# Kernel optimization log

Hardware: AMD Instinct MI355X
Metric: run time of the kernel (lower is better)

Reference implementation:

```python
import jax, jax.numpy as jnp
import numpy as np

B, R, T, Q = 4096, 130, 200, 64  # batch, ROIs, BOLD length (= feature_nums), query dim
EPS = 1e-5
GCN_DIMS = [(T, 16), (16, 16), (16, 4), (4, 4), (4, 2), (2, 2)]


def bn1d(x, g, b):
    # torch.nn.BatchNorm1d(R) on (B, R, L): channel dim=1, training-mode batch stats, biased var
    m = x.mean(axis=(0, 2), keepdims=True)
    v = ((x - m) ** 2).mean(axis=(0, 2), keepdims=True)
    return g[None, :, None] * (x - m) * jax.lax.rsqrt(v + EPS) + b[None, :, None]


def setup_inputs() -> dict:
    key = jax.random.key(0)
    ks = jax.random.split(key, 16)

    def kaiming(k, shape, fan_in):  # kaiming_normal_ with relu gain
        return (jax.random.normal(k, shape) * np.sqrt(2.0 / fan_in)).astype(jnp.float32)

    inp = {}
    inp['BOLD_signals'] = jax.random.normal(ks[0], (B, R, T), dtype=jnp.float32)
    inp['threshold'] = jnp.float32(0.005)
    inp['wq'] = kaiming(ks[1], (Q, T), T)
    inp['bq'] = jnp.zeros((Q,), jnp.float32)
    inp['g_t'] = jnp.ones((R,), jnp.float32)
    inp['b_t'] = jnp.zeros((R,), jnp.float32)
    for i, (fi, fo) in enumerate(GCN_DIMS, 1):
        inp[f'w{i}'] = kaiming(ks[1 + i], (fo, fi), fi)
        inp[f'b{i}'] = jnp.zeros((fo,), jnp.float32)
        inp[f'g{i}'] = jnp.ones((R,), jnp.float32)
        inp[f'beta{i}'] = jnp.zeros((R,), jnp.float32)
    inp['w_mlp'] = kaiming(ks[9], (2, R * 2), R * 2)
    inp['b_mlp'] = jnp.zeros((2,), jnp.float32)
    return inp


def reference(BOLD_signals, threshold, wq, bq, g_t, b_t,
              w1, b1, g1, beta1, w2, b2, g2, beta2, w3, b3, g3, beta3,
              w4, b4, g4, beta4, w5, b5, g5, beta5, w6, b6, g6, beta6,
              w_mlp, b_mlp):
    x = jnp.where(jnp.isnan(BOLD_signals), 0.0, BOLD_signals)  # (B,R,T)

    # Transformer-style relation matrix (note: K is a reshape, not a transpose, per source)
    qk = x @ wq.T + bq                      # (B,R,Q)
    Qm = qk.reshape(-1, R, Q)               # (B,R,Q)
    Km = qk.reshape(-1, Q, R)               # (B,Q,R)  -- faithful reshape
    rel = jnp.einsum('brq,bqs->brs', Qm, Km)  # (B,R,R)
    rel = bn1d(rel, g_t, b_t)
    rel = jax.nn.softmax(rel, axis=2)
    rel = jax.nn.relu(rel - threshold)

    def gcn(A, f, w, b, g, beta):
        return jax.nn.relu(bn1d(A @ f @ w.T + b, g, beta))

    h = gcn(rel, x, w1, b1, g1, beta1)           # (B,R,16)
    h = gcn(rel, h, w2, b2, g2, beta2) + h       # res
    h = gcn(rel, h, w3, b3, g3, beta3)           # (B,R,4)
    h = gcn(rel, h, w4, b4, g4, beta4) + h       # res
    h = gcn(rel, h, w5, b5, g5, beta5)           # (B,R,2)
    h = gcn(rel, h, w6, b6, g6, beta6) + h       # res

    out = jax.nn.relu(h.reshape(h.shape[0], -1) @ w_mlp.T + b_mlp)  # (B,2)
    return out
```

## Files before the change

### kernel.cpp

```cpp
#include <hip/hip_runtime.h>
#include <math.h>


typedef _Float16 f16;
typedef _Float16 f16x8 __attribute__((ext_vector_type(8)));
typedef _Float16 f16x4 __attribute__((ext_vector_type(4)));
typedef float f32x4 __attribute__((ext_vector_type(4)));

#define MFMA16(a, b, c) __builtin_amdgcn_mfma_f32_16x16x32_f16((a), (b), (c), 0, 0, 0)

__global__ __launch_bounds__(256) void k_in(
    const float* __restrict__ x, const float* __restrict__ wq,
    const float* __restrict__ w1, const float* __restrict__ bq,
    f16* __restrict__ qk, f16* __restrict__ xw1)
{
  __shared__ f16 xs[64 * 224];
  __shared__ f16 ws[80 * 224];
  const int tid = threadIdx.x;
  const size_t m0 = (size_t)blockIdx.x * 64;
  for (int i = tid; i < 192; i += 256) {
    int r = i / 3, j = i - (i / 3) * 3;
    *(float4*)&xs[r * 224 + 200 + j * 8] = make_float4(0, 0, 0, 0);
  }
  for (int i = tid; i < 240; i += 256) {
    int r = i / 3, j = i - (i / 3) * 3;
    *(float4*)&ws[r * 224 + 200 + j * 8] = make_float4(0, 0, 0, 0);
  }
  const float4* xsrc = (const float4*)(x + m0 * 200);
  for (int i = tid; i < 3200; i += 256) {
    int r = i / 50, c = i - (i / 50) * 50;
    float4 v = xsrc[i];
    v.x = (v.x != v.x) ? 0.f : v.x;
    v.y = (v.y != v.y) ? 0.f : v.y;
    v.z = (v.z != v.z) ? 0.f : v.z;
    v.w = (v.w != v.w) ? 0.f : v.w;
    f16x4 h; h[0] = (f16)v.x; h[1] = (f16)v.y; h[2] = (f16)v.z; h[3] = (f16)v.w;
    *(f16x4*)&xs[r * 224 + c * 4] = h;
  }
  for (int i = tid; i < 4000; i += 256) {
    int f = i / 50, c = i - (i / 50) * 50;
    const float4* src = (f < 64) ? (const float4*)(wq + f * 200) + c
                                 : (const float4*)(w1 + (f - 64) * 200) + c;
    float4 v = *src;
    f16x4 h; h[0] = (f16)v.x; h[1] = (f16)v.y; h[2] = (f16)v.z; h[3] = (f16)v.w;
    *(f16x4*)&ws[f * 224 + c * 4] = h;
  }
  __syncthreads();
  const int lane = tid & 63, wv = tid >> 6;
  const int mrow = lane & 15, quad = lane >> 4;
  f32x4 acc[5];
#pragma unroll
  for (int n = 0; n < 5; n++) acc[n] = (f32x4){0.f, 0.f, 0.f, 0.f};
  const f16* xrow = &xs[(wv * 16 + mrow) * 224 + quad * 8];
#pragma unroll
  for (int k0 = 0; k0 < 224; k0 += 32) {
    f16x8 af = *(const f16x8*)(xrow + k0);
#pragma unroll
    for (int n = 0; n < 5; n++) {
      f16x8 bf = *(const f16x8*)&ws[(n * 16 + mrow) * 224 + k0 + quad * 8];
      acc[n] = MFMA16(af, bf, acc[n]);
    }
  }
  const size_t rbase = m0 + wv * 16;
#pragma unroll
  for (int n = 0; n < 4; n++) {
    int col = n * 16 + mrow;
    float bqv = bq[col];
#pragma unroll
    for (int i = 0; i < 4; i++)
      qk[(rbase + quad * 4 + i) * 64 + col] = (f16)(acc[n][i] + bqv);
  }
#pragma unroll
  for (int i = 0; i < 4; i++)
    xw1[(rbase + quad * 4 + i) * 16 + mrow] = (f16)acc[4][i];
}

__device__ __forceinline__ void stage_qkt(const f16* qb, f16* Qm, f16* Kt, int tid)
{
  for (int i = tid; i < 1040; i += 256) {
    int r = i >> 3, j = i & 7;
    *(f16x8*)&Qm[r * 72 + j * 8] = *(const f16x8*)(qb + i * 8);
  }
  for (int i = tid; i < 126; i += 256) {
    int r = 130 + i / 9, j = i - (i / 9) * 9;
    *(float4*)&Qm[r * 72 + j * 8] = make_float4(0, 0, 0, 0);
    *(float4*)&Kt[r * 72 + j * 8] = make_float4(0, 0, 0, 0);
  }
  for (int i = tid; i < 8320; i += 256) {
    int q = i / 130, s = i - (i / 130) * 130;
    Kt[s * 72 + q] = qb[i];
  }
}

__global__ __launch_bounds__(256) void k_relstats(
    const f16* __restrict__ qk, float* __restrict__ sp)
{
  __shared__ f16 Qm[144 * 72];
  __shared__ f16 Kt[144 * 72];
  const int b = blockIdx.x, tid = threadIdx.x;
  stage_qkt(qk + (size_t)b * 8320, Qm, Kt, tid);
  __syncthreads();
  const int lane = tid & 63, wv = tid >> 6, mrow = lane & 15, quad = lane >> 4;
  for (int m = wv; m < 9; m += 4) {
    float p1[4] = {0, 0, 0, 0}, p2[4] = {0, 0, 0, 0};
    const f16* arow = &Qm[(m * 16 + mrow) * 72 + quad * 8];
    f16x8 af0 = *(const f16x8*)arow;
    f16x8 af1 = *(const f16x8*)(arow + 32);
    for (int n = 0; n < 9; n++) {
      const f16* brow = &Kt[(n * 16 + mrow) * 72 + quad * 8];
      f32x4 acc = (f32x4){0.f, 0.f, 0.f, 0.f};
      acc = MFMA16(af0, *(const f16x8*)brow, acc);
      acc = MFMA16(af1, *(const f16x8*)(brow + 32), acc);
#pragma unroll
      for (int i = 0; i < 4; i++) { float v = acc[i]; p1[i] += v; p2[i] += v * v; }
    }
#pragma unroll
    for (int i = 0; i < 4; i++)
#pragma unroll
      for (int msk = 1; msk <= 8; msk <<= 1) {
        p1[i] += __shfl_xor(p1[i], msk); p2[i] += __shfl_xor(p2[i], msk);
      }
    if (mrow == 0) {
#pragma unroll
      for (int i = 0; i < 4; i++) {
        int r = m * 16 + quad * 4 + i;
        if (r < 130) {
          sp[(size_t)r * 4096 + b] = p1[i];
          sp[130 * 4096 + (size_t)r * 4096 + b] = p2[i];
        }
      }
    }
  }
}

__global__ __launch_bounds__(256) void k_stats(
    const float* __restrict__ sp, const float* __restrict__ g,
    const float* __restrict__ beta, float invN, float* __restrict__ ac)
{
  const int r = blockIdx.x, tid = threadIdx.x;
  float s1 = 0.f, s2 = 0.f;
  const float* p1 = sp + (size_t)r * 4096;
  const float* p2 = sp + 130 * 4096 + (size_t)r * 4096;
  for (int j = tid; j < 4096; j += 256) { s1 += p1[j]; s2 += p2[j]; }
#pragma unroll
  for (int m = 1; m <= 32; m <<= 1) { s1 += __shfl_xor(s1, m); s2 += __shfl_xor(s2, m); }
  __shared__ float r1[4], r2[4];
  if ((tid & 63) == 0) { r1[tid >> 6] = s1; r2[tid >> 6] = s2; }
  __syncthreads();
  if (tid == 0) {
    float S1 = r1[0] + r1[1] + r1[2] + r1[3];
    float S2 = r2[0] + r2[1] + r2[2] + r2[3];
    float mean = S1 * invN;
    float var = S2 * invN - mean * mean;
    float a = g[r] * rsqrtf(var + 1e-5f);
    ac[r] = a;
    ac[130 + r] = beta[r] - mean * a;
  }
}

__global__ __launch_bounds__(256) void k_Asoft(
    const f16* __restrict__ qk, const float* __restrict__ ac0,
    const float* __restrict__ thrp, f16* __restrict__ A16)
{
  __shared__ f16 Qm[144 * 72];
  __shared__ f16 Kt[144 * 72];
  const int b = blockIdx.x, tid = threadIdx.x;
  stage_qkt(qk + (size_t)b * 8320, Qm, Kt, tid);
  __syncthreads();
  const float thr = *thrp;
  const int lane = tid & 63, wv = tid >> 6, mrow = lane & 15, quad = lane >> 4;
  f16* Ab = A16 + (size_t)b * 17680;
  for (int m = wv; m < 9; m += 4) {
    float a4[4], c4[4];
#pragma unroll
    for (int i = 0; i < 4; i++) {
      int r = m * 16 + quad * 4 + i;
      a4[i] = (r < 130) ? ac0[r] : 0.f;
      c4[i] = (r < 130) ? ac0[130 + r] : 0.f;
    }
    const f16* arow = &Qm[(m * 16 + mrow) * 72 + quad * 8];
    f16x8 af0 = *(const f16x8*)arow;
    f16x8 af1 = *(const f16x8*)(arow + 32);
    float mx[4] = {-3e38f, -3e38f, -3e38f, -3e38f}, sm[4] = {0, 0, 0, 0};
    for (int n = 0; n < 9; n++) {
      const f16* brow = &Kt[(n * 16 + mrow) * 72 + quad * 8];
      f32x4 acc = (f32x4){0.f, 0.f, 0.f, 0.f};
      acc = MFMA16(af0, *(const f16x8*)brow, acc);
      acc = MFMA16(af1, *(const f16x8*)(brow + 32), acc);
      const bool valid = (n * 16 + mrow) < 130;
#pragma unroll
      for (int i = 0; i < 4; i++) {
        float v = a4[i] * acc[i] + c4[i];
        float ve = valid ? v : -3e38f;
        float nm = fmaxf(mx[i], ve);
        sm[i] = sm[i] * __expf(mx[i] - nm) + (valid ? __expf(v - nm) : 0.f);
        mx[i] = nm;
      }
    }
#pragma unroll
    for (int i = 0; i < 4; i++) {
#pragma unroll
      for (int msk = 1; msk <= 8; msk <<= 1) {
        float om = __shfl_xor(mx[i], msk), os = __shfl_xor(sm[i], msk);
        float nm = fmaxf(mx[i], om);
        sm[i] = sm[i] * __expf(mx[i] - nm) + os * __expf(om - nm);
        mx[i] = nm;
      }
      sm[i] = 1.f / sm[i];
    }
    for (int n = 0; n < 9; n++) {
      const f16* brow = &Kt[(n * 16 + mrow) * 72 + quad * 8];
      f32x4 acc = (f32x4){0.f, 0.f, 0.f, 0.f};
      acc = MFMA16(af0, *(const f16x8*)brow, acc);
      acc = MFMA16(af1, *(const f16x8*)(brow + 32), acc);
      const int col = n * 16 + mrow;
#pragma unroll
      for (int i = 0; i < 4; i++) {
        int r = m * 16 + quad * 4 + i;
        if (r < 130) {
          if (col < 130) {
            float v = a4[i] * acc[i] + c4[i];
            float Av = fmaxf(__expf(v - mx[i]) * sm[i] - thr, 0.f);
            Ab[r * 136 + col] = (f16)Av;
          } else if (col < 136) {
            Ab[r * 136 + col] = (f16)0.f;
          }
        }
      }
    }
  }
}

template <int FI, int FO, bool RES, bool G1>
__global__ __launch_bounds__(256) void k_gcn(
    const f16* __restrict__ A16, const float* __restrict__ ZP,
    const float* __restrict__ ZQ, const f16* __restrict__ xw1,
    const float* __restrict__ acP, const float* __restrict__ acQ,
    const float* __restrict__ wmat, const float* __restrict__ bb,
    float* __restrict__ Zout, float* __restrict__ sp)
{
  __shared__ f16 Ald[144 * 160];
  __shared__ f16 gT[16 * 160];
  const int b = blockIdx.x, tid = threadIdx.x;
  const f16* Ab = A16 + (size_t)b * 17680;
  for (int i = tid; i < 2210; i += 256) {
    int r = i / 17, c8 = i - (i / 17) * 17;
    *(f16x8*)&Ald[r * 160 + c8 * 8] = *(const f16x8*)(Ab + r * 136 + c8 * 8);
  }
  for (int i = tid; i < 432; i += 256) {
    int r = i / 3, j = i - (i / 3) * 3;
    *(float4*)&Ald[r * 160 + 136 + j * 8] = make_float4(0, 0, 0, 0);
  }
  for (int i = tid; i < 320; i += 256)
    ((float4*)gT)[i] = make_float4(0, 0, 0, 0);
  __syncthreads();
  if constexpr (G1) {
    for (int i = tid; i < 2080; i += 256) {
      int s = i >> 4, f = i & 15;
      gT[f * 160 + s] = xw1[(size_t)b * 2080 + i];
    }
  } else {
    if (tid < 130) {
      const int r = tid;
      float h[FI];
      const float* zp = ZP + ((size_t)b * 130 + r) * FI;
      const float aP = acP[r], cP = acP[130 + r];
#pragma unroll
      for (int i = 0; i < FI; i++) h[i] = fmaxf(aP * zp[i] + cP, 0.f);
      if constexpr (RES) {
        const float* zq = ZQ + ((size_t)b * 130 + r) * FI;
        const float aQ = acQ[r], cQ = acQ[130 + r];
#pragma unroll
        for (int i = 0; i < FI; i++) h[i] += fmaxf(aQ * zq[i] + cQ, 0.f);
      }
#pragma unroll
      for (int k = 0; k < FO; k++) {
        float s = 0.f;
#pragma unroll
        for (int i = 0; i < FI; i++) s += h[i] * wmat[k * FI + i];
        gT[k * 160 + r] = (f16)s;
      }
    }
  }
  __syncthreads();
  const int lane = tid & 63, wv = tid >> 6, mrow = lane & 15, quad = lane >> 4;
  for (int m = wv; m < 9; m += 4) {
    f32x4 acc = (f32x4){0.f, 0.f, 0.f, 0.f};
    const f16* arow = &Ald[(m * 16 + mrow) * 160];
    const f16* brow = &gT[mrow * 160];
#pragma unroll
    for (int k0 = 0; k0 < 160; k0 += 32) {
      f16x8 af = *(const f16x8*)(arow + k0 + quad * 8);
      f16x8 bf = *(const f16x8*)(brow + k0 + quad * 8);
      acc = MFMA16(af, bf, acc);
    }
    const int col = mrow;
    const float bk = (col < FO) ? bb[col] : 0.f;
    float p1[4], p2[4];
#pragma unroll
    for (int i = 0; i < 4; i++) {
      int r = m * 16 + quad * 4 + i;
      float v = (col < FO) ? acc[i] + bk : 0.f;
      if (col < FO && r < 130)
        Zout[((size_t)b * 130 + r) * FO + col] = v;
      p1[i] = v; p2[i] = v * v;
    }
#pragma unroll
    for (int i = 0; i < 4; i++)
#pragma unroll
      for (int msk = 1; msk <= 8; msk <<= 1) {
        p1[i] += __shfl_xor(p1[i], msk); p2[i] += __shfl_xor(p2[i], msk);
      }
    if (mrow == 0) {
#pragma unroll
      for (int i = 0; i < 4; i++) {
        int r = m * 16 + quad * 4 + i;
        if (r < 130) {
          sp[(size_t)r * 4096 + b] = p1[i];
          sp[130 * 4096 + (size_t)r * 4096 + b] = p2[i];
        }
      }
    }
  }
}

__global__ __launch_bounds__(256) void k_mlp(
    const float* __restrict__ Z5, const float* __restrict__ Z6,
    const float* __restrict__ ac5, const float* __restrict__ ac6,
    const float* __restrict__ wm, const float* __restrict__ bm, float* __restrict__ out)
{
  const int tid = threadIdx.x, lane = tid & 63, wv = tid >> 6;
  const int b = blockIdx.x * 4 + wv;
  const float* z5 = Z5 + (size_t)b * 260;
  const float* z6 = Z6 + (size_t)b * 260;
  float p0 = 0.f, p1 = 0.f;
#pragma unroll
  for (int j = 0; j < 5; j++) {
    int i = lane + 64 * j;
    if (i < 260) {
      int r = i >> 1;
      float h = fmaxf(ac6[r] * z6[i] + ac6[130 + r], 0.f)
              + fmaxf(ac5[r] * z5[i] + ac5[130 + r], 0.f);
      p0 += h * wm[i];
      p1 += h * wm[260 + i];
    }
  }
#pragma unroll
  for (int m = 1; m <= 32; m <<= 1) { p0 += __shfl_xor(p0, m); p1 += __shfl_xor(p1, m); }
  if (lane == 0) {
    out[(size_t)b * 2] = fmaxf(p0 + bm[0], 0.f);
    out[(size_t)b * 2 + 1] = fmaxf(p1 + bm[1], 0.f);
  }
}

extern "C" void kernel_launch(void* const* d_in, const int* in_sizes, int n_in,
                              void* d_out, int out_size, void* d_ws, size_t ws_size,
                              hipStream_t stream) {
  const float* X   = (const float*)d_in[0];
  const float* THR = (const float*)d_in[1];
  const float* WQ  = (const float*)d_in[2];
  const float* BQ  = (const float*)d_in[3];
  const float* GT  = (const float*)d_in[4];
  const float* BT  = (const float*)d_in[5];
  const float* W1 = (const float*)d_in[6];  const float* Bb1 = (const float*)d_in[7];
  const float* G1g = (const float*)d_in[8]; const float* BE1 = (const float*)d_in[9];
  const float* W2 = (const float*)d_in[10]; const float* Bb2 = (const float*)d_in[11];
  const float* G2 = (const float*)d_in[12]; const float* BE2 = (const float*)d_in[13];
  const float* W3 = (const float*)d_in[14]; const float* Bb3 = (const float*)d_in[15];
  const float* G3 = (const float*)d_in[16]; const float* BE3 = (const float*)d_in[17];
  const float* W4 = (const float*)d_in[18]; const float* Bb4 = (const float*)d_in[19];
  const float* G4 = (const float*)d_in[20]; const float* BE4 = (const float*)d_in[21];
  const float* W5 = (const float*)d_in[22]; const float* Bb5 = (const float*)d_in[23];
  const float* G5 = (const float*)d_in[24]; const float* BE5 = (const float*)d_in[25];
  const float* W6 = (const float*)d_in[26]; const float* Bb6 = (const float*)d_in[27];
  const float* G6 = (const float*)d_in[28]; const float* BE6 = (const float*)d_in[29];
  const float* WM = (const float*)d_in[30]; const float* BM = (const float*)d_in[31];

  float* ws = (float*)d_ws;
  f16*   A16   = (f16*)ws;
  f16*   qk16  = (f16*)(ws + 36208640);
  f16*   xw116 = (f16*)(ws + 53248000);
  float* Z1 = ws + 57507840;
  float* Z2 = ws + 66027520;
  float* Z3 = ws + 74547200;
  float* Z4 = ws + 76677120;
  float* Z5 = ws + 78807040;
  float* Z6 = ws + 79872000;
  float* sp = ws + 80936960;
  float* ac = ws + 82001920;

  k_in<<<8320, 256, 0, stream>>>(X, WQ, W1, BQ, qk16, xw116);
  k_relstats<<<4096, 256, 0, stream>>>(qk16, sp);
  k_stats<<<130, 256, 0, stream>>>(sp, GT, BT, 1.f / 532480.f, ac);
  k_Asoft<<<4096, 256, 0, stream>>>(qk16, ac, THR, A16);
  k_gcn<16, 16, false, true><<<4096, 256, 0, stream>>>(A16, nullptr, nullptr, xw116,
      nullptr, nullptr, nullptr, Bb1, Z1, sp);
  k_stats<<<130, 256, 0, stream>>>(sp, G1g, BE1, 1.f / 65536.f, ac + 260);
  k_gcn<16, 16, false, false><<<4096, 256, 0, stream>>>(A16, Z1, nullptr, nullptr,
      ac + 260, nullptr, W2, Bb2, Z2, sp);
  k_stats<<<130, 256, 0, stream>>>(sp, G2, BE2, 1.f / 65536.f, ac + 520);
  k_gcn<16, 4, true, false><<<4096, 256, 0, stream>>>(A16, Z2, Z1, nullptr,
      ac + 520, ac + 260, W3, Bb3, Z3, sp);
  k_stats<<<130, 256, 0, stream>>>(sp, G3, BE3, 1.f / 16384.f, ac + 780);
  k_gcn<4, 4, false, false><<<4096, 256, 0, stream>>>(A16, Z3, nullptr, nullptr,
      ac + 780, nullptr, W4, Bb4, Z4, sp);
  k_stats<<<130, 256, 0, stream>>>(sp, G4, BE4, 1.f / 16384.f, ac + 1040);
  k_gcn<4, 2, true, false><<<4096, 256, 0, stream>>>(A16, Z4, Z3, nullptr,
      ac + 1040, ac + 780, W5, Bb5, Z5, sp);
  k_stats<<<130, 256, 0, stream>>>(sp, G5, BE5, 1.f / 8192.f, ac + 1300);
  k_gcn<2, 2, false, false><<<4096, 256, 0, stream>>>(A16, Z5, nullptr, nullptr,
      ac + 1300, nullptr, W6, Bb6, Z6, sp);
  k_stats<<<130, 256, 0, stream>>>(sp, G6, BE6, 1.f / 8192.f, ac + 1560);
  k_mlp<<<1024, 256, 0, stream>>>(Z5, Z6, ac + 1300, ac + 1560, WM, BM, (float*)d_out);
}
```

Baseline: 1.248 ms.

## Pre-convert weights once, drop redundant LDS staging across kernels

```diff
diff --git a/kernel.cpp b/kernel.cpp
--- a/kernel.cpp
+++ b/kernel.cpp
@@ -9,22 +9,28 @@
 
 #define MFMA16(a, b, c) __builtin_amdgcn_mfma_f32_16x16x32_f16((a), (b), (c), 0, 0, 0)
 
+__global__ __launch_bounds__(256) void w_prep(
+    const float* __restrict__ wq, const float* __restrict__ w1, f16* __restrict__ wf)
+{
+  const int f = blockIdx.x;
+  const int k = threadIdx.x;
+  if (k < 224) {
+    float v = 0.f;
+    if (k < 200) v = (f < 64) ? wq[f * 200 + k] : w1[(f - 64) * 200 + k];
+    wf[f * 224 + k] = (f16)v;
+  }
+}
+
 __global__ __launch_bounds__(256) void k_in(
-    const float* __restrict__ x, const float* __restrict__ wq,
-    const float* __restrict__ w1, const float* __restrict__ bq,
-    f16* __restrict__ qk, f16* __restrict__ xw1)
-{
-  __shared__ f16 xs[64 * 224];
-  __shared__ f16 ws[80 * 224];
+    const float* __restrict__ x, const f16* __restrict__ wf,
+    const float* __restrict__ bq, f16* __restrict__ qk, f16* __restrict__ xw1)
+{
+  __shared__ f16 xs[64 * 232];
   const int tid = threadIdx.x;
   const size_t m0 = (size_t)blockIdx.x * 64;
-  for (int i = tid; i < 192; i += 256) {
-    int r = i / 3, j = i - (i / 3) * 3;
-    *(float4*)&xs[r * 224 + 200 + j * 8] = make_float4(0, 0, 0, 0);
-  }
-  for (int i = tid; i < 240; i += 256) {
-    int r = i / 3, j = i - (i / 3) * 3;
-    *(float4*)&ws[r * 224 + 200 + j * 8] = make_float4(0, 0, 0, 0);
+  {
+    int r = tid >> 2, j = tid & 3;
+    *(float4*)&xs[r * 232 + 200 + j * 8] = make_float4(0, 0, 0, 0);
   }
   const float4* xsrc = (const float4*)(x + m0 * 200);
   for (int i = tid; i < 3200; i += 256) {
@@ -35,15 +41,7 @@
     v.z = (v.z != v.z) ? 0.f : v.z;
     v.w = (v.w != v.w) ? 0.f : v.w;
     f16x4 h; h[0] = (f16)v.x; h[1] = (f16)v.y; h[2] = (f16)v.z; h[3] = (f16)v.w;
-    *(f16x4*)&xs[r * 224 + c * 4] = h;
-  }
-  for (int i = tid; i < 4000; i += 256) {
-    int f = i / 50, c = i - (i / 50) * 50;
-    const float4* src = (f < 64) ? (const float4*)(wq + f * 200) + c
-                                 : (const float4*)(w1 + (f - 64) * 200) + c;
-    float4 v = *src;
-    f16x4 h; h[0] = (f16)v.x; h[1] = (f16)v.y; h[2] = (f16)v.z; h[3] = (f16)v.w;
-    *(f16x4*)&ws[f * 224 + c * 4] = h;
+    *(f16x4*)&xs[r * 232 + c * 4] = h;
   }
   __syncthreads();
   const int lane = tid & 63, wv = tid >> 6;
@@ -51,15 +49,14 @@
   f32x4 acc[5];
 #pragma unroll
   for (int n = 0; n < 5; n++) acc[n] = (f32x4){0.f, 0.f, 0.f, 0.f};
-  const f16* xrow = &xs[(wv * 16 + mrow) * 224 + quad * 8];
+  const f16* xrow = &xs[(wv * 16 + mrow) * 232 + quad * 8];
+  const f16* wrow = wf + mrow * 224 + quad * 8;
 #pragma unroll
   for (int k0 = 0; k0 < 224; k0 += 32) {
     f16x8 af = *(const f16x8*)(xrow + k0);
 #pragma unroll
-    for (int n = 0; n < 5; n++) {
-      f16x8 bf = *(const f16x8*)&ws[(n * 16 + mrow) * 224 + k0 + quad * 8];
-      acc[n] = MFMA16(af, bf, acc[n]);
-    }
+    for (int n = 0; n < 5; n++)
+      acc[n] = MFMA16(af, *(const f16x8*)(wrow + n * 3584 + k0), acc[n]);
   }
   const size_t rbase = m0 + wv * 16;
 #pragma unroll
@@ -75,42 +72,48 @@
     xw1[(rbase + quad * 4 + i) * 16 + mrow] = (f16)acc[4][i];
 }
 
-__device__ __forceinline__ void stage_qkt(const f16* qb, f16* Qm, f16* Kt, int tid)
-{
-  for (int i = tid; i < 1040; i += 256) {
-    int r = i >> 3, j = i & 7;
-    *(f16x8*)&Qm[r * 72 + j * 8] = *(const f16x8*)(qb + i * 8);
-  }
-  for (int i = tid; i < 126; i += 256) {
-    int r = 130 + i / 9, j = i - (i / 9) * 9;
-    *(float4*)&Qm[r * 72 + j * 8] = make_float4(0, 0, 0, 0);
-    *(float4*)&Kt[r * 72 + j * 8] = make_float4(0, 0, 0, 0);
-  }
-  for (int i = tid; i < 8320; i += 256) {
-    int q = i / 130, s = i - (i / 130) * 130;
-    Kt[s * 72 + q] = qb[i];
+__device__ __forceinline__ void gather_bfrags(const f16* qf, int mrow, int quad,
+                                              f16x8 bf[9][2])
+{
+#pragma unroll
+  for (int n = 0; n < 9; n++) {
+    const int s = n * 16 + mrow;
+    const bool ok = (s < 130);
+#pragma unroll
+    for (int kh = 0; kh < 2; kh++) {
+      f16x8 t;
+#pragma unroll
+      for (int j = 0; j < 8; j++) {
+        int q = kh * 32 + quad * 8 + j;
+        t[j] = ok ? qf[q * 130 + s] : (f16)0.f;
+      }
+      bf[n][kh] = t;
+    }
   }
 }
 
 __global__ __launch_bounds__(256) void k_relstats(
     const f16* __restrict__ qk, float* __restrict__ sp)
 {
-  __shared__ f16 Qm[144 * 72];
-  __shared__ f16 Kt[144 * 72];
+  __shared__ f16 qf[8320];
   const int b = blockIdx.x, tid = threadIdx.x;
-  stage_qkt(qk + (size_t)b * 8320, Qm, Kt, tid);
+  const f16* qb = qk + (size_t)b * 8320;
+  for (int i = tid; i < 1040; i += 256)
+    *(f16x8*)&qf[i * 8] = *(const f16x8*)(qb + i * 8);
   __syncthreads();
   const int lane = tid & 63, wv = tid >> 6, mrow = lane & 15, quad = lane >> 4;
+  f16x8 bf[9][2];
+  gather_bfrags(qf, mrow, quad, bf);
   for (int m = wv; m < 9; m += 4) {
-    float p1[4] = {0, 0, 0, 0}, p2[4] = {0, 0, 0, 0};
-    const f16* arow = &Qm[(m * 16 + mrow) * 72 + quad * 8];
+    const f16* arow = qb + (m * 16 + mrow) * 64 + quad * 8;
     f16x8 af0 = *(const f16x8*)arow;
     f16x8 af1 = *(const f16x8*)(arow + 32);
+    float p1[4] = {0, 0, 0, 0}, p2[4] = {0, 0, 0, 0};
+#pragma unroll
     for (int n = 0; n < 9; n++) {
-      const f16* brow = &Kt[(n * 16 + mrow) * 72 + quad * 8];
       f32x4 acc = (f32x4){0.f, 0.f, 0.f, 0.f};
-      acc = MFMA16(af0, *(const f16x8*)brow, acc);
-      acc = MFMA16(af1, *(const f16x8*)(brow + 32), acc);
+      acc = MFMA16(af0, bf[n][0], acc);
+      acc = MFMA16(af1, bf[n][1], acc);
 #pragma unroll
       for (int i = 0; i < 4; i++) { float v = acc[i]; p1[i] += v; p2[i] += v * v; }
     }
@@ -162,13 +165,16 @@
     const f16* __restrict__ qk, const float* __restrict__ ac0,
     const float* __restrict__ thrp, f16* __restrict__ A16)
 {
-  __shared__ f16 Qm[144 * 72];
-  __shared__ f16 Kt[144 * 72];
+  __shared__ f16 qf[8320];
   const int b = blockIdx.x, tid = threadIdx.x;
-  stage_qkt(qk + (size_t)b * 8320, Qm, Kt, tid);
+  const f16* qb = qk + (size_t)b * 8320;
+  for (int i = tid; i < 1040; i += 256)
+    *(f16x8*)&qf[i * 8] = *(const f16x8*)(qb + i * 8);
   __syncthreads();
   const float thr = *thrp;
   const int lane = tid & 63, wv = tid >> 6, mrow = lane & 15, quad = lane >> 4;
+  f16x8 bf[9][2];
+  gather_bfrags(qf, mrow, quad, bf);
   f16* Ab = A16 + (size_t)b * 17680;
   for (int m = wv; m < 9; m += 4) {
     float a4[4], c4[4];
@@ -178,19 +184,23 @@
       a4[i] = (r < 130) ? ac0[r] : 0.f;
       c4[i] = (r < 130) ? ac0[130 + r] : 0.f;
     }
-    const f16* arow = &Qm[(m * 16 + mrow) * 72 + quad * 8];
+    const f16* arow = qb + (m * 16 + mrow) * 64 + quad * 8;
     f16x8 af0 = *(const f16x8*)arow;
     f16x8 af1 = *(const f16x8*)(arow + 32);
+    f32x4 acc[9];
+#pragma unroll
+    for (int n = 0; n < 9; n++) {
+      acc[n] = (f32x4){0.f, 0.f, 0.f, 0.f};
+      acc[n] = MFMA16(af0, bf[n][0], acc[n]);
+      acc[n] = MFMA16(af1, bf[n][1], acc[n]);
+    }
     float mx[4] = {-3e38f, -3e38f, -3e38f, -3e38f}, sm[4] = {0, 0, 0, 0};
+#pragma unroll
     for (int n = 0; n < 9; n++) {
-      const f16* brow = &Kt[(n * 16 + mrow) * 72 + quad * 8];
-      f32x4 acc = (f32x4){0.f, 0.f, 0.f, 0.f};
-      acc = MFMA16(af0, *(const f16x8*)brow, acc);
-      acc = MFMA16(af1, *(const f16x8*)(brow + 32), acc);
       const bool valid = (n * 16 + mrow) < 130;
 #pragma unroll
       for (int i = 0; i < 4; i++) {
-        float v = a4[i] * acc[i] + c4[i];
+        float v = a4[i] * acc[n][i] + c4[i];
         float ve = valid ? v : -3e38f;
         float nm = fmaxf(mx[i], ve);
         sm[i] = sm[i] * __expf(mx[i] - nm) + (valid ? __expf(v - nm) : 0.f);
@@ -208,20 +218,16 @@
       }
       sm[i] = 1.f / sm[i];
     }
+#pragma unroll
     for (int n = 0; n < 9; n++) {
-      const f16* brow = &Kt[(n * 16 + mrow) * 72 + quad * 8];
-      f32x4 acc = (f32x4){0.f, 0.f, 0.f, 0.f};
-      acc = MFMA16(af0, *(const f16x8*)brow, acc);
-      acc = MFMA16(af1, *(const f16x8*)(brow + 32), acc);
       const int col = n * 16 + mrow;
 #pragma unroll
       for (int i = 0; i < 4; i++) {
         int r = m * 16 + quad * 4 + i;
         if (r < 130) {
           if (col < 130) {
-            float v = a4[i] * acc[i] + c4[i];
-            float Av = fmaxf(__expf(v - mx[i]) * sm[i] - thr, 0.f);
-            Ab[r * 136 + col] = (f16)Av;
+            float v = a4[i] * acc[n][i] + c4[i];
+            Ab[r * 136 + col] = (f16)fmaxf(__expf(v - mx[i]) * sm[i] - thr, 0.f);
           } else if (col < 136) {
             Ab[r * 136 + col] = (f16)0.f;
           }
@@ -239,25 +245,14 @@
     const float* __restrict__ wmat, const float* __restrict__ bb,
     float* __restrict__ Zout, float* __restrict__ sp)
 {
-  __shared__ f16 Ald[144 * 160];
-  __shared__ f16 gT[16 * 160];
+  __shared__ f16 gT[16 * 168];
   const int b = blockIdx.x, tid = threadIdx.x;
-  const f16* Ab = A16 + (size_t)b * 17680;
-  for (int i = tid; i < 2210; i += 256) {
-    int r = i / 17, c8 = i - (i / 17) * 17;
-    *(f16x8*)&Ald[r * 160 + c8 * 8] = *(const f16x8*)(Ab + r * 136 + c8 * 8);
-  }
-  for (int i = tid; i < 432; i += 256) {
-    int r = i / 3, j = i - (i / 3) * 3;
-    *(float4*)&Ald[r * 160 + 136 + j * 8] = make_float4(0, 0, 0, 0);
-  }
-  for (int i = tid; i < 320; i += 256)
-    ((float4*)gT)[i] = make_float4(0, 0, 0, 0);
+  for (int i = tid; i < 1344; i += 256) ((float*)gT)[i] = 0.f;
   __syncthreads();
   if constexpr (G1) {
     for (int i = tid; i < 2080; i += 256) {
       int s = i >> 4, f = i & 15;
-      gT[f * 160 + s] = xw1[(size_t)b * 2080 + i];
+      gT[f * 168 + s] = xw1[(size_t)b * 2080 + i];
     }
   } else {
     if (tid < 130) {
@@ -278,22 +273,23 @@
         float s = 0.f;
 #pragma unroll
         for (int i = 0; i < FI; i++) s += h[i] * wmat[k * FI + i];
-        gT[k * 160 + r] = (f16)s;
+        gT[k * 168 + r] = (f16)s;
       }
     }
   }
   __syncthreads();
   const int lane = tid & 63, wv = tid >> 6, mrow = lane & 15, quad = lane >> 4;
+  f16x8 bfr[5];
+#pragma unroll
+  for (int kk = 0; kk < 5; kk++)
+    bfr[kk] = *(const f16x8*)&gT[mrow * 168 + kk * 32 + quad * 8];
+  const f16* Ab = A16 + (size_t)b * 17680;
   for (int m = wv; m < 9; m += 4) {
+    const f16* arow = Ab + (m * 16 + mrow) * 136 + quad * 8;
     f32x4 acc = (f32x4){0.f, 0.f, 0.f, 0.f};
-    const f16* arow = &Ald[(m * 16 + mrow) * 160];
-    const f16* brow = &gT[mrow * 160];
-#pragma unroll
-    for (int k0 = 0; k0 < 160; k0 += 32) {
-      f16x8 af = *(const f16x8*)(arow + k0 + quad * 8);
-      f16x8 bf = *(const f16x8*)(brow + k0 + quad * 8);
-      acc = MFMA16(af, bf, acc);
-    }
+#pragma unroll
+    for (int kk = 0; kk < 5; kk++)
+      acc = MFMA16(*(const f16x8*)(arow + kk * 32), bfr[kk], acc);
     const int col = mrow;
     const float bk = (col < FO) ? bb[col] : 0.f;
     float p1[4], p2[4];
@@ -380,16 +376,18 @@
   f16*   A16   = (f16*)ws;
   f16*   qk16  = (f16*)(ws + 36208640);
   f16*   xw116 = (f16*)(ws + 53248000);
-  float* Z1 = ws + 57507840;
-  float* Z2 = ws + 66027520;
-  float* Z3 = ws + 74547200;
-  float* Z4 = ws + 76677120;
-  float* Z5 = ws + 78807040;
-  float* Z6 = ws + 79872000;
-  float* sp = ws + 80936960;
-  float* ac = ws + 82001920;
-
-  k_in<<<8320, 256, 0, stream>>>(X, WQ, W1, BQ, qk16, xw116);
+  f16*   wf16  = (f16*)(ws + 57507840);
+  float* Z1 = ws + 57516800;
+  float* Z2 = ws + 66036480;
+  float* Z3 = ws + 74556160;
+  float* Z4 = ws + 76686080;
+  float* Z5 = ws + 78816000;
+  float* Z6 = ws + 79880960;
+  float* sp = ws + 80945920;
+  float* ac = ws + 82010880;
+
+  w_prep<<<80, 256, 0, stream>>>(WQ, W1, wf16);
+  k_in<<<8320, 256, 0, stream>>>(X, wf16, BQ, qk16, xw116);
   k_relstats<<<4096, 256, 0, stream>>>(qk16, sp);
   k_stats<<<130, 256, 0, stream>>>(sp, GT, BT, 1.f / 532480.f, ac);
   k_Asoft<<<4096, 256, 0, stream>>>(qk16, ac, THR, A16);
```

After: 1.134 ms. -9.1%, faster.
